# Kernel tuning notes

Hardware: AMD Instinct MI355X
Metric: run time of the kernel (lower is better)

Reference implementation:

```python
import jax, jax.numpy as jnp
import numpy as np

GAMMA = 0.9
SCALE_BASE = 512.0


def _xpos(x, downscale=False):
    """XPOS rotary embedding (torchscale variant) applied to x: (B, L, D)."""
    B, L, D = x.shape
    half = D // 2
    # per-channel magnitude base: ((2i) + 0.4*D) / (1.4*D), i over even channels
    scale_vec = (jnp.arange(0, D, 2, dtype=jnp.float32) + 0.4 * D) / (1.4 * D)  # (half,)
    power = jnp.arange(L, dtype=jnp.float32) / SCALE_BASE                        # (L,)
    scale = scale_vec[None, :] ** power[:, None]                                 # (L, half)
    if downscale:
        scale = 1.0 / scale
    # fixed sinusoidal frequencies over `half` dims
    inv_freq = 1.0 / (10000.0 ** (jnp.arange(half, dtype=jnp.float32) / half))   # (half,)
    sinusoid = jnp.arange(L, dtype=jnp.float32)[:, None] * inv_freq[None, :]     # (L, half)
    sin = jnp.repeat(jnp.sin(sinusoid) * scale, 2, axis=-1)                      # (L, D) interleaved dup
    cos = jnp.repeat(jnp.cos(sinusoid) * scale, 2, axis=-1)
    # rotate_every_two: (x0,x1,x2,x3,...) -> (-x1,x0,-x3,x2,...)
    x_even = x[..., 0::2]
    x_odd = x[..., 1::2]
    rot = jnp.stack((-x_odd, x_even), axis=-1).reshape(x.shape)
    return x * cos + rot * sin


def _get_D(seq_len):
    n = jnp.arange(seq_len, dtype=jnp.float32)[:, None]
    m = jnp.arange(seq_len, dtype=jnp.float32)[None, :]
    D = GAMMA ** jnp.abs(n - m)  # non-causal decay, no NaNs since gamma > 0
    return D


def setup_inputs() -> dict:
    key = jax.random.key(0)
    k1, k2, k3, k4 = jax.random.split(key, 4)
    B, L, H, Dh = 8, 2048, 1024, 1024
    X = jax.random.normal(k1, (B, L, H), dtype=jnp.float32)
    W_Q = jax.random.normal(k2, (H, Dh), dtype=jnp.float32) / H
    W_K = jax.random.normal(k3, (H, Dh), dtype=jnp.float32) / H
    W_V = jax.random.normal(k4, (H, Dh), dtype=jnp.float32) / H
    return {"X": X, "W_Q": W_Q, "W_K": W_K, "W_V": W_V}


def reference(X, W_Q, W_K, W_V):
    B, L, H = X.shape
    D = _get_D(L)                       # (L, L)
    Q = _xpos(X @ W_Q)                  # (B, L, Dh)
    K = _xpos(X @ W_K, downscale=True)  # (B, L, Dh)
    V = X @ W_V                         # (B, L, Dv)
    scores = jnp.einsum('bqd,bkd->bqk', Q, K)   # (B, L, L)
    p_attn = jax.nn.softmax(scores, axis=-1)
    p_attn = p_attn * D[None, :, :]              # elementwise decay AFTER softmax
    return jnp.einsum('bqk,bkv->bqv', p_attn, V)
```

## Files before the change

kernel.cpp:

```cpp
#include <hip/hip_runtime.h>
#include <math.h>


#define LDIM 2048
#define HDIM 1024
#define MTOT 16384

typedef unsigned short u16;
typedef unsigned int u32;
typedef __attribute__((ext_vector_type(16))) float f32x16;
typedef __attribute__((ext_vector_type(8))) short s16x8;

#define GLD16(gp, lp) __builtin_amdgcn_global_load_lds( \
    (const __attribute__((address_space(1))) void*)(gp), \
    (__attribute__((address_space(3))) void*)(lp), 16, 0, 0)

__device__ __forceinline__ u16 f2bf(float f) {
    unsigned u = __float_as_uint(f);
    return (u16)((u + 0x7FFFu + ((u >> 16) & 1u)) >> 16);
}

__device__ __forceinline__ void sincos_rev(float ang, float* sn, float* cs) {
    double dr = (double)ang * 0.15915494309189535;
    dr -= __builtin_floor(dr);
    float fr = (float)dr;
    float s_, c_;
    asm("v_sin_f32 %0, %1" : "=v"(s_) : "v"(fr));
    asm("v_cos_f32 %0, %1" : "=v"(c_) : "v"(fr));
    *sn = s_; *cs = c_;
}

#define ROW32(reg, laneHi) (((reg) & 3) + 8 * ((reg) >> 2) + 4 * (laneHi))

__device__ __forceinline__ void gemm256(const u16* __restrict__ A,
                                        const u16* __restrict__ B,
                                        int lda, int ldb, int K, int m0, int n0,
                                        char* smem, int tid, f32x16 (*acc)[2])
{
    const int wv = tid >> 6, ln = tid & 63;
    const int wm = wv >> 2, wn = wv & 3;
    const int lane31 = ln & 31, laneHi = ln >> 5;
    const int srow = tid >> 3;
    const int scol = ((tid & 7) ^ (srow & 7)) * 8;

    const u16* ap[4];
    const u16* bp[4];
#pragma unroll
    for (int r = 0; r < 4; ++r) {
        ap[r] = A + (size_t)(m0 + r * 64 + srow) * lda + scol;
        bp[r] = B + (size_t)(n0 + r * 64 + srow) * ldb + scol;
    }

    int abyte[4], bbyte[2];
    const int slot_r = (laneHi ^ (lane31 & 7)) << 4;
#pragma unroll
    for (int fm = 0; fm < 4; ++fm)
        abyte[fm] = (wm * 128 + fm * 32 + lane31) * 128 + slot_r;
#pragma unroll
    for (int fn = 0; fn < 2; ++fn)
        bbyte[fn] = 32768 + (wn * 64 + fn * 32 + lane31) * 128 + slot_r;

#define STAGE256(sl) do {                                                  \
        char* d_ = smem + (sl) * 65536;                                    \
        _Pragma("unroll")                                                  \
        for (int r_ = 0; r_ < 4; ++r_) {                                   \
            GLD16(ap[r_], d_ + r_ * 8192 + tid * 16);                      \
            ap[r_] += 64;                                                  \
        }                                                                  \
        _Pragma("unroll")                                                  \
        for (int r_ = 0; r_ < 4; ++r_) {                                   \
            GLD16(bp[r_], d_ + 32768 + r_ * 8192 + tid * 16);              \
            bp[r_] += 64;                                                  \
        }                                                                  \
    } while (0)

    const int nk = K >> 6;
    STAGE256(0);
    __syncthreads();

    int buf = 0;
#pragma unroll 1
    for (int t = 0; t < nk; ++t) {
        if (t + 1 < nk) STAGE256(buf ^ 1);
        const char* Bb = smem + buf * 65536;
#pragma unroll
        for (int ks = 0; ks < 4; ++ks) {
            s16x8 af[4], bf[2];
#pragma unroll
            for (int fm = 0; fm < 4; ++fm)
                af[fm] = *(const s16x8*)(Bb + (abyte[fm] ^ (ks << 5)));
#pragma unroll
            for (int fn = 0; fn < 2; ++fn)
                bf[fn] = *(const s16x8*)(Bb + (bbyte[fn] ^ (ks << 5)));
#pragma unroll
            for (int fm = 0; fm < 4; ++fm)
#pragma unroll
                for (int fn = 0; fn < 2; ++fn)
                    acc[fm][fn] = __builtin_amdgcn_mfma_f32_32x32x16_bf16(
                        af[fm], bf[fn], acc[fm][fn], 0, 0, 0);
        }
        __syncthreads();
        buf ^= 1;
    }
#undef STAGE256
}

__global__ __launch_bounds__(256) void gen_tab(u32* __restrict__ CSq,
                                               u32* __restrict__ CSk)
{
    const int l = blockIdx.x;
    for (int ih = threadIdx.x; ih < 512; ih += 256) {
        float invf = exp2f(-13.287712379549449f * (1.f / 512.f) * (float)ih);
        float sn, cs;
        sincos_rev((float)l * invf, &sn, &cs);
        float l2sv = log2f(((float)(2 * ih) + 409.6f) * (1.f / 1433.6f));
        float e = (float)l * (1.f / 512.f) * l2sv;
        float sq = exp2f(e), sk = exp2f(-e);
        CSq[l * 512 + ih] = (u32)f2bf(cs * sq) | ((u32)f2bf(sn * sq) << 16);
        CSk[l * 512 + ih] = (u32)f2bf(cs * sk) | ((u32)f2bf(sn * sk) << 16);
    }
}

__global__ __launch_bounds__(256) void cast_x(const float* __restrict__ X,
                                              u16* __restrict__ Xb, int n4)
{
    int i = blockIdx.x * 256 + threadIdx.x;
    const int stride = gridDim.x * 256;
    for (; i < n4; i += stride) {
        float4 v = ((const float4*)X)[i];
        ushort4 o = make_ushort4(f2bf(v.x), f2bf(v.y), f2bf(v.z), f2bf(v.w));
        ((ushort4*)Xb)[i] = o;
    }
}

__global__ __launch_bounds__(256) void transw(const float* __restrict__ Wq,
                                              const float* __restrict__ Wk,
                                              const float* __restrict__ Wv,
                                              u16* __restrict__ WT)
{
    __shared__ float L[64][65];
    const int z = blockIdx.z;
    const float* Wz = (z == 0) ? Wq : (z == 1) ? Wk : Wv;
    u16* Oz = WT + (size_t)z * HDIM * HDIM;
    const int k0 = blockIdx.y * 64, n0 = blockIdx.x * 64;
    const int t = threadIdx.x;
    const int r_ = t >> 4, c4 = (t & 15) * 4;
#pragma unroll
    for (int it = 0; it < 4; ++it) {
        const int row = it * 16 + r_;
        float4 v = *(const float4*)&Wz[(size_t)(k0 + row) * HDIM + n0 + c4];
        L[row][c4 + 0] = v.x; L[row][c4 + 1] = v.y;
        L[row][c4 + 2] = v.z; L[row][c4 + 3] = v.w;
    }
    __syncthreads();
#pragma unroll
    for (int it = 0; it < 4; ++it) {
        const int orow = it * 16 + r_;
        ushort4 o = make_ushort4(f2bf(L[c4 + 0][orow]), f2bf(L[c4 + 1][orow]),
                                 f2bf(L[c4 + 2][orow]), f2bf(L[c4 + 3][orow]));
        *(ushort4*)&Oz[(size_t)(n0 + orow) * HDIM + k0 + c4] = o;
    }
}

__global__ __launch_bounds__(512, 2) void qkv_gemm(
    const u16* __restrict__ Xb, const u16* __restrict__ WT,
    const u32* __restrict__ CSq, const u32* __restrict__ CSk,
    u16* __restrict__ Qb, u16* __restrict__ Kb, u16* __restrict__ Vt)
{
    __shared__ __align__(16) char smem[256 * 264 * 2];
    const int bid = blockIdx.x;
    const int xcd = bid & 7, t = bid >> 3;
    const int m8 = t & 7;
    const int n_ = (t >> 3) & 3;
    const int z  = t >> 5;
    const int m0 = (xcd * 8 + m8) * 256;
    const int n0 = n_ * 256;
    const int tid = threadIdx.x;

    f32x16 acc[4][2] = {};

    gemm256(Xb, WT + (size_t)z * HDIM * HDIM, HDIM, HDIM, HDIM, m0, n0, smem, tid, acc);

    const int wv = tid >> 6, ln = tid & 63;
    const int wm = wv >> 2, wn = wv & 3;
    const int lane31 = ln & 31, laneHi = ln >> 5;
    const int l0 = m0 & (LDIM - 1);
    u16* T = (u16*)smem;

    if (z < 2) {
        const u32* CS = (z == 0) ? CSq : CSk;
#pragma unroll
        for (int fn = 0; fn < 2; ++fn) {
            const int gc = n0 + wn * 64 + fn * 32 + lane31;
            const int ih = gc >> 1;
            const float sgn = (gc & 1) ? 1.f : -1.f;
            const u32* tb = CS + (size_t)l0 * 512 + ih;
#pragma unroll
            for (int fm = 0; fm < 4; ++fm) {
#pragma unroll
                for (int reg = 0; reg < 16; ++reg) {
                    const int rowl = wm * 128 + fm * 32 + ROW32(reg, laneHi);
                    u32 v = tb[(size_t)rowl * 512];
                    float cs = __uint_as_float(v << 16);
                    float sn = __uint_as_float(v & 0xFFFF0000u);
                    float c = acc[fm][fn][reg];
                    float p = __shfl_xor(c, 1);
                    T[rowl * 264 + wn * 64 + fn * 32 + lane31] =
                        f2bf(c * cs + sgn * p * sn);
                }
            }
        }
        __syncthreads();
        u16* Out = (z == 0) ? Qb : Kb;
        const int row_ = tid >> 5, slot = tid & 31;
#pragma unroll
        for (int g = 0; g < 16; ++g) {
            const int row = g * 16 + row_;
            s16x8 v = *(const s16x8*)&T[row * 264 + slot * 8];
            *(s16x8*)&Out[(size_t)(m0 + row) * HDIM + n0 + slot * 8] = v;
        }
    } else {
#pragma unroll
        for (int fn = 0; fn < 2; ++fn)
#pragma unroll
            for (int fm = 0; fm < 4; ++fm)
#pragma unroll
                for (int reg = 0; reg < 16; ++reg)
                    T[(wn * 64 + fn * 32 + lane31) * 264 +
                      wm * 128 + fm * 32 + ROW32(reg, laneHi)] =
                        f2bf(acc[fm][fn][reg]);
        __syncthreads();
        const int b = m0 >> 11;
        const int row_ = tid >> 5, slot = tid & 31;
#pragma unroll
        for (int g = 0; g < 16; ++g) {
            const int row = g * 16 + row_;
            s16x8 v = *(const s16x8*)&T[row * 264 + slot * 8];
            *(s16x8*)&Vt[((size_t)b * HDIM + n0 + row) * LDIM + l0 + slot * 8] = v;
        }
    }
}

__global__ __launch_bounds__(512, 2) void qk_gemm(
    const u16* __restrict__ Q, const u16* __restrict__ Km,
    u16* __restrict__ Wm, float* __restrict__ Zp)
{
    __shared__ __align__(16) char smem[256 * 264 * 2];
    __shared__ float Zl[4][256];
    const int bid = blockIdx.x;
    const int b = bid & 7, t = bid >> 3;
    const int mt = t & 7;
    const int nt = t >> 3;
    const int m0 = mt * 256;
    const int n0 = nt * 256;
    const int tid = threadIdx.x;

    f32x16 acc[4][2] = {};

    gemm256(Q + (size_t)b * LDIM * HDIM, Km + (size_t)b * LDIM * HDIM,
            HDIM, HDIM, HDIM, m0, n0, smem, tid, acc);

    const int wv = tid >> 6, ln = tid & 63;
    const int wm = wv >> 2, wn = wv & 3;
    const int lane31 = ln & 31, laneHi = ln >> 5;
    u16* T = (u16*)smem;
    const float LOG2E = 1.4426950408889634f;
    const float LOG2G = -0.15200309344504997f;

#pragma unroll
    for (int fm = 0; fm < 4; ++fm) {
        float ps[16];
#pragma unroll
        for (int reg = 0; reg < 16; ++reg) ps[reg] = 0.f;
#pragma unroll
        for (int fn = 0; fn < 2; ++fn) {
            const int gk = n0 + wn * 64 + fn * 32 + lane31;
#pragma unroll
            for (int reg = 0; reg < 16; ++reg) {
                const int mloc = wm * 128 + fm * 32 + ROW32(reg, laneHi);
                const int gq = m0 + mloc;
                float t1 = acc[fm][fn][reg] * LOG2E;
                float e = exp2f(t1);
                int dd = gq - gk; dd = dd < 0 ? -dd : dd;
                ps[reg] += e;
                T[mloc * 264 + wn * 64 + fn * 32 + lane31] =
                    f2bf(exp2f(t1 + (float)dd * LOG2G));
            }
        }
#pragma unroll
        for (int reg = 0; reg < 16; ++reg) {
            float s = ps[reg];
            s += __shfl_xor(s, 1); s += __shfl_xor(s, 2);
            s += __shfl_xor(s, 4); s += __shfl_xor(s, 8);
            s += __shfl_xor(s, 16);
            if (lane31 == 0)
                Zl[wn][wm * 128 + fm * 32 + ROW32(reg, laneHi)] = s;
        }
    }
    __syncthreads();

    const int row_ = tid >> 5, slot = tid & 31;
#pragma unroll
    for (int g = 0; g < 16; ++g) {
        const int row = g * 16 + row_;
        s16x8 v = *(const s16x8*)&T[row * 264 + slot * 8];
        *(s16x8*)&Wm[((size_t)b * LDIM + m0 + row) * LDIM + n0 + slot * 8] = v;
    }
    if (tid < 256)
        Zp[((size_t)b * 8 + nt) * LDIM + m0 + tid] =
            Zl[0][tid] + Zl[1][tid] + Zl[2][tid] + Zl[3][tid];
}

__global__ __launch_bounds__(512, 2) void pv_gemm(
    const u16* __restrict__ Wm, const u16* __restrict__ Vt,
    const float* __restrict__ Zp, float* __restrict__ Out)
{
    __shared__ __align__(16) char smem[2 * 65536];
    __shared__ float Zinv[256];
    const int bid = blockIdx.x;
    const int b = bid & 7, t = bid >> 3;
    const int mt4 = t & 3;
    const int nt = (t >> 2) & 3;
    const int mtH = t >> 4;
    const int m0 = (mtH * 4 + mt4) * 256;
    const int n0 = nt * 256;
    const int tid = threadIdx.x;

    if (tid < 256) {
        float zz = 0.f;
#pragma unroll
        for (int nb = 0; nb < 8; ++nb)
            zz += Zp[((size_t)b * 8 + nb) * LDIM + m0 + tid];
        Zinv[tid] = 1.0f / zz;
    }

    f32x16 acc[4][2] = {};

    gemm256(Wm + (size_t)b * LDIM * LDIM, Vt + (size_t)b * HDIM * LDIM,
            LDIM, LDIM, LDIM, m0, n0, smem, tid, acc);

    const int wv = tid >> 6, ln = tid & 63;
    const int wm = wv >> 2, wn = wv & 3;
    const int lane31 = ln & 31, laneHi = ln >> 5;
    float* Ob = Out + (size_t)b * LDIM * HDIM;
#pragma unroll
    for (int fm = 0; fm < 4; ++fm)
#pragma unroll
        for (int fn = 0; fn < 2; ++fn) {
            const int gn = n0 + wn * 64 + fn * 32 + lane31;
#pragma unroll
            for (int reg = 0; reg < 16; ++reg) {
                const int row = wm * 128 + fm * 32 + ROW32(reg, laneHi);
                Ob[(size_t)(m0 + row) * HDIM + gn] = acc[fm][fn][reg] * Zinv[row];
            }
        }
}

extern "C" void kernel_launch(void* const* d_in, const int* in_sizes, int n_in,
                              void* d_out, int out_size, void* d_ws, size_t ws_size,
                              hipStream_t stream)
{
    (void)in_sizes; (void)n_in; (void)out_size; (void)ws_size;
    const float* X  = (const float*)d_in[0];
    const float* Wq = (const float*)d_in[1];
    const float* Wk = (const float*)d_in[2];
    const float* Wv = (const float*)d_in[3];
    char* ws = (char*)d_ws;
    const size_t MB = 1024 * 1024;

    u16* Wmat = (u16*)ws;
    u16* Xb   = (u16*)ws;
    u16* WT   = (u16*)(ws + 32 * MB);
    u16* Qb   = (u16*)(ws + 64 * MB);
    u16* Kb   = (u16*)(ws + 96 * MB);
    u16* Vt   = (u16*)(ws + 128 * MB);
    float* Zp = (float*)(ws + 160 * MB);
    u32* CSq  = (u32*)(ws + 161 * MB);
    u32* CSk  = (u32*)(ws + 165 * MB);

    gen_tab<<<2048, 256, 0, stream>>>(CSq, CSk);
    cast_x<<<2048, 256, 0, stream>>>(X, Xb, MTOT * HDIM / 4);
    transw<<<dim3(16, 16, 3), 256, 0, stream>>>(Wq, Wk, Wv, WT);
    qkv_gemm<<<768, 512, 0, stream>>>(Xb, WT, CSq, CSk, Qb, Kb, Vt);
    qk_gemm<<<512, 512, 0, stream>>>(Qb, Kb, Wmat, Zp);
    pv_gemm<<<256, 512, 0, stream>>>(Wmat, Vt, Zp, (float*)d_out);
}
```

Measured before the change: 325.9 us.

## Pipeline GEMM mainloop with half-tile staging, split waits and MFMA priority

Rewrites the shared 256x256 bf16 GEMM mainloop. K=64 tiles are now split into two 32-wide halves stored as separate LDS blocks with a 4-slot XOR swizzle. Global-to-LDS loads for the next tile are interleaved between the LDS reads and MFMA groups, using explicit vmcnt waits and barriers instead of one __syncthreads per tile. MFMA bursts are wrapped in s_setprio so other waves can keep issuing loads. A barrier is also added after the Zinv setup in the PV kernel, now required because the initial full-tile sync is gone; the gain is finer-grained overlap at the cost of more barriers per iteration.

```diff
diff --git a/kernel.cpp b/kernel.cpp
--- a/kernel.cpp
+++ b/kernel.cpp
@@ -32,77 +32,93 @@
 
 #define ROW32(reg, laneHi) (((reg) & 3) + 8 * ((reg) >> 2) + 4 * (laneHi))
 
-__device__ __forceinline__ void gemm256(const u16* __restrict__ A,
-                                        const u16* __restrict__ B,
-                                        int lda, int ldb, int K, int m0, int n0,
-                                        char* smem, int tid, f32x16 (*acc)[2])
+__device__ __forceinline__ void gemm256p(const u16* __restrict__ A,
+                                         const u16* __restrict__ B,
+                                         int lda, int ldb, int K, int m0, int n0,
+                                         char* smem, int tid, f32x16 (*acc)[2])
 {
     const int wv = tid >> 6, ln = tid & 63;
     const int wm = wv >> 2, wn = wv & 3;
     const int lane31 = ln & 31, laneHi = ln >> 5;
-    const int srow = tid >> 3;
-    const int scol = ((tid & 7) ^ (srow & 7)) * 8;
-
-    const u16* ap[4];
-    const u16* bp[4];
-#pragma unroll
-    for (int r = 0; r < 4; ++r) {
-        ap[r] = A + (size_t)(m0 + r * 64 + srow) * lda + scol;
-        bp[r] = B + (size_t)(n0 + r * 64 + srow) * ldb + scol;
-    }
-
-    int abyte[4], bbyte[2];
-    const int slot_r = (laneHi ^ (lane31 & 7)) << 4;
-#pragma unroll
-    for (int fm = 0; fm < 4; ++fm)
-        abyte[fm] = (wm * 128 + fm * 32 + lane31) * 128 + slot_r;
-#pragma unroll
-    for (int fn = 0; fn < 2; ++fn)
-        bbyte[fn] = 32768 + (wn * 64 + fn * 32 + lane31) * 128 + slot_r;
-
-#define STAGE256(sl) do {                                                  \
-        char* d_ = smem + (sl) * 65536;                                    \
-        _Pragma("unroll")                                                  \
-        for (int r_ = 0; r_ < 4; ++r_) {                                   \
-            GLD16(ap[r_], d_ + r_ * 8192 + tid * 16);                      \
-            ap[r_] += 64;                                                  \
-        }                                                                  \
-        _Pragma("unroll")                                                  \
-        for (int r_ = 0; r_ < 4; ++r_) {                                   \
-            GLD16(bp[r_], d_ + 32768 + r_ * 8192 + tid * 16);              \
-            bp[r_] += 64;                                                  \
-        }                                                                  \
+
+    const int srow = tid >> 2;
+    const int scol = ((tid & 3) ^ (srow & 3)) * 8;
+    const u16* ap0 = A + (size_t)(m0 + srow) * lda + scol;
+    const u16* ap1 = A + (size_t)(m0 + 128 + srow) * lda + scol;
+    const u16* bp0 = B + (size_t)(n0 + srow) * ldb + scol;
+    const u16* bp1 = B + (size_t)(n0 + 128 + srow) * ldb + scol;
+    int ak = 0, bk = 0;
+
+    int arb[4], ar3[4];
+#pragma unroll
+    for (int fm = 0; fm < 4; ++fm) {
+        const int r = wm * 128 + fm * 32 + lane31;
+        arb[fm] = r * 64; ar3[fm] = r & 3;
+    }
+    int brb[2], br3[2];
+#pragma unroll
+    for (int fn = 0; fn < 2; ++fn) {
+        const int r = wn * 64 + fn * 32 + lane31;
+        brb[fn] = r * 64; br3[fn] = r & 3;
+    }
+
+#define STAGE_A(blk) do { char* d_ = smem + (blk) * 16384 + tid * 16;         \
+        GLD16(ap0 + ak, d_); GLD16(ap1 + ak, d_ + 8192); ak += 32; } while (0)
+#define STAGE_B(blk) do { char* d_ = smem + 65536 + (blk) * 16384 + tid * 16; \
+        GLD16(bp0 + bk, d_); GLD16(bp1 + bk, d_ + 8192); bk += 32; } while (0)
+
+#define READS(d, ks, af, bf) do {                                             \
+        const char* Ab_ = smem + ((d) * 2 + ((ks) >> 1)) * 16384;             \
+        const char* Bb_ = Ab_ + 65536;                                        \
+        const int sl_ = (((ks) & 1) << 1) | laneHi;                           \
+        _Pragma("unroll") for (int fm_ = 0; fm_ < 4; ++fm_)                   \
+            af[fm_] = *(const s16x8*)(Ab_ + arb[fm_] + ((sl_ ^ ar3[fm_]) << 4)); \
+        _Pragma("unroll") for (int fn_ = 0; fn_ < 2; ++fn_)                   \
+            bf[fn_] = *(const s16x8*)(Bb_ + brb[fn_] + ((sl_ ^ br3[fn_]) << 4)); \
     } while (0)
 
+#define MFMA8(af, bf) do {                                                    \
+        __builtin_amdgcn_s_setprio(1);                                        \
+        _Pragma("unroll") for (int fm_ = 0; fm_ < 4; ++fm_)                   \
+            _Pragma("unroll") for (int fn_ = 0; fn_ < 2; ++fn_)               \
+                acc[fm_][fn_] = __builtin_amdgcn_mfma_f32_32x32x16_bf16(      \
+                    af[fm_], bf[fn_], acc[fm_][fn_], 0, 0, 0);                \
+        __builtin_amdgcn_s_setprio(0);                                        \
+    } while (0)
+
+#define WAITBAR(n) do {                                                      \
+        asm volatile("s_waitcnt vmcnt(" #n ")" ::: "memory");                 \
+        __builtin_amdgcn_s_barrier();                                         \
+        __builtin_amdgcn_sched_barrier(0); } while (0)
+
     const int nk = K >> 6;
-    STAGE256(0);
+
+    STAGE_A(0); STAGE_B(0); STAGE_A(1); STAGE_B(1);
+    WAITBAR(4);
+
+#pragma unroll 1
+    for (int t = 0; t < nk - 1; ++t) {
+        const int d = t & 1, e = d ^ 1;
+        s16x8 af[4], bf[2];
+        READS(d, 0, af, bf); STAGE_A(e * 2 + 0);            MFMA8(af, bf);
+        READS(d, 1, af, bf); STAGE_B(e * 2 + 0); WAITBAR(4); MFMA8(af, bf);
+        READS(d, 2, af, bf); STAGE_A(e * 2 + 1);            MFMA8(af, bf);
+        READS(d, 3, af, bf); STAGE_B(e * 2 + 1); WAITBAR(4); MFMA8(af, bf);
+    }
+    {
+        const int d = (nk - 1) & 1;
+        s16x8 af[4], bf[2];
+        READS(d, 0, af, bf);              MFMA8(af, bf);
+        READS(d, 1, af, bf); WAITBAR(0);  MFMA8(af, bf);
+        READS(d, 2, af, bf);              MFMA8(af, bf);
+        READS(d, 3, af, bf);              MFMA8(af, bf);
+    }
     __syncthreads();
-
-    int buf = 0;
-#pragma unroll 1
-    for (int t = 0; t < nk; ++t) {
-        if (t + 1 < nk) STAGE256(buf ^ 1);
-        const char* Bb = smem + buf * 65536;
-#pragma unroll
-        for (int ks = 0; ks < 4; ++ks) {
-            s16x8 af[4], bf[2];
-#pragma unroll
-            for (int fm = 0; fm < 4; ++fm)
-                af[fm] = *(const s16x8*)(Bb + (abyte[fm] ^ (ks << 5)));
-#pragma unroll
-            for (int fn = 0; fn < 2; ++fn)
-                bf[fn] = *(const s16x8*)(Bb + (bbyte[fn] ^ (ks << 5)));
-#pragma unroll
-            for (int fm = 0; fm < 4; ++fm)
-#pragma unroll
-                for (int fn = 0; fn < 2; ++fn)
-                    acc[fm][fn] = __builtin_amdgcn_mfma_f32_32x32x16_bf16(
-                        af[fm], bf[fn], acc[fm][fn], 0, 0, 0);
-        }
-        __syncthreads();
-        buf ^= 1;
-    }
-#undef STAGE256
+#undef STAGE_A
+#undef STAGE_B
+#undef READS
+#undef MFMA8
+#undef WAITBAR
 }
 
 __global__ __launch_bounds__(256) void gen_tab(u32* __restrict__ CSq,
@@ -179,7 +195,7 @@
 
     f32x16 acc[4][2] = {};
 
-    gemm256(Xb, WT + (size_t)z * HDIM * HDIM, HDIM, HDIM, HDIM, m0, n0, smem, tid, acc);
+    gemm256p(Xb, WT + (size_t)z * HDIM * HDIM, HDIM, HDIM, HDIM, m0, n0, smem, tid, acc);
 
     const int wv = tid >> 6, ln = tid & 63;
     const int wm = wv >> 2, wn = wv & 3;
@@ -257,8 +273,8 @@
 
     f32x16 acc[4][2] = {};
 
-    gemm256(Q + (size_t)b * LDIM * HDIM, Km + (size_t)b * LDIM * HDIM,
-            HDIM, HDIM, HDIM, m0, n0, smem, tid, acc);
+    gemm256p(Q + (size_t)b * LDIM * HDIM, Km + (size_t)b * LDIM * HDIM,
+             HDIM, HDIM, HDIM, m0, n0, smem, tid, acc);
 
     const int wv = tid >> 6, ln = tid & 63;
     const int wm = wv >> 2, wn = wv & 3;
@@ -333,11 +349,12 @@
             zz += Zp[((size_t)b * 8 + nb) * LDIM + m0 + tid];
         Zinv[tid] = 1.0f / zz;
     }
+    __syncthreads();
 
     f32x16 acc[4][2] = {};
 
-    gemm256(Wm + (size_t)b * LDIM * LDIM, Vt + (size_t)b * HDIM * LDIM,
-            LDIM, LDIM, LDIM, m0, n0, smem, tid, acc);
+    gemm256p(Wm + (size_t)b * LDIM * LDIM, Vt + (size_t)b * HDIM * LDIM,
+             LDIM, LDIM, LDIM, m0, n0, smem, tid, acc);
 
     const int wv = tid >> 6, ln = tid & 63;
     const int wm = wv >> 2, wn = wv & 3;
```

Measured after the change: 347.3 us. +6.6%, slower.
